# Kernel optimization log

Hardware: AMD Instinct MI355X
Metric: run time of the kernel (lower is better)

The kernel has to match this reference:

```python
import jax, jax.numpy as jnp
import numpy as np
import math

B, TQ, TK, D, H, K = 4, 1024, 1536, 1024, 16, 1
DV = D // H * K  # 64
DP = D * K       # projection dim


def setup_inputs() -> dict:
    key = jax.random.key(0)
    ks = jax.random.split(key, 12)
    s = 0.02
    query = jax.random.normal(ks[0], (B, TQ, D), dtype=jnp.float32)
    key_value = jax.random.normal(ks[1], (B, TK, D), dtype=jnp.float32)
    relative = jax.random.normal(ks[2], (B, TK, D), dtype=jnp.float32)
    # Transformer-XL causal mask: query i may attend to key j <= i + mem
    mem = TK - TQ
    i = jnp.arange(TQ)[:, None]
    j = jnp.arange(TK)[None, :]
    mask = jnp.broadcast_to(j > i + mem, (B, TQ, TK))  # True = masked
    Wq = jax.random.normal(ks[3], (D, DP), dtype=jnp.float32) * s
    Wk = jax.random.normal(ks[4], (D, DP), dtype=jnp.float32) * s
    Wv = jax.random.normal(ks[5], (D, DP), dtype=jnp.float32) * s
    Wr = jax.random.normal(ks[6], (D, DP), dtype=jnp.float32) * s
    Wo = jax.random.normal(ks[7], (DP, D), dtype=jnp.float32) * s
    u = jax.random.normal(ks[8], (DV,), dtype=jnp.float32) * s
    v = jax.random.normal(ks[9], (DV,), dtype=jnp.float32) * s
    gamma = jnp.ones((D,), dtype=jnp.float32)
    beta = jnp.zeros((D,), dtype=jnp.float32)
    return {"query": query, "key_value": key_value, "relative": relative,
            "mask": mask, "Wq": Wq, "Wk": Wk, "Wv": Wv, "Wr": Wr, "Wo": Wo,
            "u": u, "v": v, "gamma": gamma, "beta": beta}


def _layer_norm(x, gamma, beta, eps=1e-5):
    mu = jnp.mean(x, axis=-1, keepdims=True)
    var = jnp.mean(jnp.square(x - mu), axis=-1, keepdims=True)
    return (x - mu) * jax.lax.rsqrt(var + eps) * gamma + beta


def reference(query, key_value, relative, mask, Wq, Wk, Wv, Wr, Wo, u, v, gamma, beta):
    b, tq, d = query.shape
    tk = key_value.shape[1]
    dv = u.shape[0]
    h = Wq.shape[1] // dv
    q = (query @ Wq).reshape(b, tq, h, dv)
    k = (key_value @ Wk).reshape(b, tk, h, dv)
    val = (key_value @ Wv).reshape(b, tk, h, dv)
    r = (relative @ Wr).reshape(b, tk, h, dv)
    # content term (q+u)K^T and position term (q+v)R^T, per head
    ac = jnp.einsum('bqhd,bkhd->bhqk', q + u, k)
    bd = jnp.einsum('bqhd,bkhd->bhqk', q + v, r)
    logits = (ac + bd) * (1.0 / math.sqrt(dv))
    logits = jnp.where(mask[:, None, :, :], -jnp.inf, logits)
    w = jax.nn.softmax(logits, axis=-1)
    ctx = jnp.einsum('bhqk,bkhd->bqhd', w, val).reshape(b, tq, h * dv)
    out = ctx @ Wo + query  # residual
    return _layer_norm(out, gamma, beta)
```

## Files before the change

### kernel.cpp

```cpp
#include <hip/hip_runtime.h>


typedef unsigned short u16;
typedef __attribute__((ext_vector_type(8))) short short8;
typedef __attribute__((ext_vector_type(4))) float floatx4;

#define ATTN_SC 0.18033688011112042f

__device__ __forceinline__ float bf2f(u16 u) {
    union { unsigned int i; float f; } w; w.i = ((unsigned int)u) << 16; return w.f;
}
__device__ __forceinline__ u16 f2bf(float f) {
    union { unsigned int i; float f; } w; w.f = f;
    unsigned int u = w.i;
    return (u16)((u + 0x7FFFu + ((u >> 16) & 1u)) >> 16);
}

__device__ __forceinline__ void gl_lds16(const u16* g, u16* lds) {
    __builtin_amdgcn_global_load_lds(
        (const __attribute__((address_space(1))) void*)g,
        (__attribute__((address_space(3))) void*)lds, 16, 0, 0);
}

__global__ __launch_bounds__(256) void cvt3_kernel(
    const float* __restrict__ x0, u16* __restrict__ y0, int n0,
    const float* __restrict__ x1, u16* __restrict__ y1, int n1,
    const float* __restrict__ x2, u16* __restrict__ y2, int n2)
{
    const int which = blockIdx.y;
    const float* x = (which == 0) ? x0 : (which == 1) ? x1 : x2;
    u16* y         = (which == 0) ? y0 : (which == 1) ? y1 : y2;
    const int n    = (which == 0) ? n0 : (which == 1) ? n1 : n2;
    const int i = (blockIdx.x * 256 + threadIdx.x) * 8;
    if (i >= n) return;
    float4 a = *(const float4*)&x[i];
    float4 b = *(const float4*)&x[i + 4];
    short8 o;
    o[0] = (short)f2bf(a.x); o[1] = (short)f2bf(a.y);
    o[2] = (short)f2bf(a.z); o[3] = (short)f2bf(a.w);
    o[4] = (short)f2bf(b.x); o[5] = (short)f2bf(b.y);
    o[6] = (short)f2bf(b.z); o[7] = (short)f2bf(b.w);
    *(short8*)&y[i] = o;
}

__global__ __launch_bounds__(256) void transpose5_kernel(
    const float* __restrict__ Wq, const float* __restrict__ Wk,
    const float* __restrict__ Wr, const float* __restrict__ Wv,
    const float* __restrict__ Wo,
    u16* __restrict__ WqT, u16* __restrict__ WkrT,
    u16* __restrict__ WvT, u16* __restrict__ WoT)
{
    const int z = blockIdx.z;
    const float* W; u16* WT; int dst_ld, dst_koff;
    switch (z) {
        case 0: W = Wq; WT = WqT;  dst_ld = 1024; dst_koff = 0;    break;
        case 1: W = Wk; WT = WkrT; dst_ld = 2048; dst_koff = 0;    break;
        case 2: W = Wr; WT = WkrT; dst_ld = 2048; dst_koff = 1024; break;
        case 3: W = Wv; WT = WvT;  dst_ld = 1024; dst_koff = 0;    break;
        default:W = Wo; WT = WoT;  dst_ld = 1024; dst_koff = 0;    break;
    }
    __shared__ u16 ts[64][72];
    const int k0 = blockIdx.x * 64, n0 = blockIdx.y * 64;
    const int r  = threadIdx.x >> 2;
    const int c4 = (threadIdx.x & 3) << 4;
    const float* src = &W[(size_t)(k0 + r) * 1024 + n0 + c4];
    for (int j = 0; j < 16; j += 4) {
        float4 a = *(const float4*)(src + j);
        ts[r][c4 + j + 0] = f2bf(a.x);
        ts[r][c4 + j + 1] = f2bf(a.y);
        ts[r][c4 + j + 2] = f2bf(a.z);
        ts[r][c4 + j + 3] = f2bf(a.w);
    }
    __syncthreads();
    short8 t0, t1;
    for (int j = 0; j < 8; j++) t0[j] = (short)ts[c4 + j][r];
    for (int j = 0; j < 8; j++) t1[j] = (short)ts[c4 + 8 + j][r];
    u16* dst = &WT[(size_t)(n0 + r) * dst_ld + dst_koff + k0 + c4];
    *(short8*)dst       = t0;
    *(short8*)(dst + 8) = t1;
}

__global__ __launch_bounds__(256) void wuv_kernel(
    const float* __restrict__ Wk, const float* __restrict__ Wr,
    const float* __restrict__ u, const float* __restrict__ v,
    u16* __restrict__ wuvb)
{
    int idx = blockIdx.x * 256 + threadIdx.x;
    int c = idx >> 4, h = idx & 15;
    float au = 0.f, av = 0.f;
    for (int d = 0; d < 64; d++) {
        au += Wk[(size_t)c * 1024 + h * 64 + d] * u[d];
        av += Wr[(size_t)c * 1024 + h * 64 + d] * v[d];
    }
    wuvb[h * 2048 + c]        = f2bf(au);
    wuvb[h * 2048 + 1024 + c] = f2bf(av);
}

template <int EPI>
__device__ __forceinline__ void gemm_body(
    const u16* __restrict__ A0, const u16* __restrict__ A1,
    const u16* __restrict__ WT, void* __restrict__ out,
    int Kld, int kbeg, int kend, int Ksplit, int T,
    int bm, int bn, u16* As, u16* Ws)
{
    const int tid = threadIdx.x;
    const int wave = tid >> 6, lane = tid & 63;
    const int wm = wave >> 1, wn = wave & 1;
    const int l16 = lane & 15, quad = lane >> 4;

    floatx4 acc[4][4];
    const floatx4 zf = {0.f, 0.f, 0.f, 0.f};
    for (int i = 0; i < 4; i++) for (int j = 0; j < 4; j++) acc[i][j] = zf;

    const int m_base = bm * 128, n_base = bn * 128;
    const int rl = lane >> 2;
    const int cl = (lane & 3) * 8;

    for (int k0 = kbeg; k0 < kend; k0 += 32) {
        const u16* Aptr; int kk;
        if (k0 < Ksplit) { Aptr = A0; kk = k0; } else { Aptr = A1; kk = k0 - Ksplit; }
        __syncthreads();
        for (int half = 0; half < 2; half++) {
            const int r = wave * 32 + half * 16;
            gl_lds16(Aptr + (size_t)(m_base + r + rl) * 1024 + kk + cl, &As[r * 32]);
            gl_lds16(WT   + (size_t)(n_base + r + rl) * Kld  + k0 + cl, &Ws[r * 32]);
        }
        __syncthreads();

        short8 af[4], bf[4];
        for (int i = 0; i < 4; i++) {
            af[i] = *(const short8*)&As[(wm * 64 + i * 16 + l16) * 32 + quad * 8];
            bf[i] = *(const short8*)&Ws[(wn * 64 + i * 16 + l16) * 32 + quad * 8];
        }
        for (int i = 0; i < 4; i++)
            for (int j = 0; j < 4; j++)
                acc[i][j] = __builtin_amdgcn_mfma_f32_16x16x32_bf16(af[i], bf[j], acc[i][j], 0, 0, 0);
    }

    for (int i = 0; i < 4; i++) {
        for (int rg = 0; rg < 4; rg++) {
            const int m = m_base + wm * 64 + i * 16 + quad * 4 + rg;
            float* op = (float*)out;
            for (int j = 0; j < 4; j++) {
                const int col = n_base + wn * 64 + j * 16 + l16;
                op[(size_t)m * 1024 + col] = acc[i][j][rg];
            }
        }
    }
}

__device__ __forceinline__ void stage_half(
    const u16* __restrict__ src, int src_ld, int row_base, int col_base,
    u16* lds_slot, int wave, int lane)
{
    const int r = wave * 16 + (lane >> 2);
    const int c = (((lane & 3) ^ ((lane >> 2) & 3)) << 3);
    gl_lds16(src + (size_t)(row_base + r) * src_ld + col_base + c,
             lds_slot + wave * 512);
    gl_lds16(src + (size_t)(row_base + 128 + r) * src_ld + col_base + c,
             lds_slot + 4096 + wave * 512);
}

template <int EPI, int T>
__device__ __forceinline__ void gemm256_body(
    const u16* __restrict__ A0, const u16* __restrict__ A1,
    const u16* __restrict__ WT, void* __restrict__ out,
    int Kld, int NT, int KsplitTile, int bm, int bn,
    u16* As, u16* Bs)
{
    const int tid  = threadIdx.x;
    const int wave = tid >> 6, lane = tid & 63;
    const int wm = wave >> 2, wn = wave & 3;
    const int l16 = lane & 15, quad = lane >> 4;
    const int m_base = bm * 256, n_base = bn * 256;

    floatx4 acc[8][4];
    const floatx4 zf = {0.f, 0.f, 0.f, 0.f};
    #pragma unroll
    for (int i = 0; i < 8; i++)
        #pragma unroll
        for (int j = 0; j < 4; j++) acc[i][j] = zf;

    {
        const u16* sa0 = (0 < KsplitTile) ? A0 : A1;
        stage_half(sa0, 1024, m_base, 0,  As + 0 * 8192, wave, lane);
        stage_half(WT,  Kld,  n_base, 0,  Bs + 0 * 8192, wave, lane);
        stage_half(sa0, 1024, m_base, 32, As + 1 * 8192, wave, lane);
        stage_half(WT,  Kld,  n_base, 32, Bs + 1 * 8192, wave, lane);
        const u16* sa1 = (1 < KsplitTile) ? A0 : A1;
        const int  c1  = (1 < KsplitTile) ? 64 : (1 - KsplitTile) * 64;
        stage_half(sa1, 1024, m_base, c1, As + 2 * 8192, wave, lane);
        stage_half(WT,  Kld,  n_base, 64, Bs + 2 * 8192, wave, lane);
    }

    for (int t = 0; t < NT; ++t) {
        if (t + 1 < NT) asm volatile("s_waitcnt vmcnt(4)" ::: "memory");
        else            asm volatile("s_waitcnt vmcnt(0)" ::: "memory");
        __builtin_amdgcn_s_barrier();

        short8 bfr[4];
        #pragma unroll
        for (int ph = 0; ph < 4; ++ph) {
            if (ph) __builtin_amdgcn_s_barrier();
            const int ks = ph >> 1, mh = ph & 1;

            if (ph == 0) {
                if (t + 1 < NT) {
                    const int tt = t + 1;
                    const u16* sa = (tt < KsplitTile) ? A0 : A1;
                    const int cb = (tt < KsplitTile ? tt : tt - KsplitTile) * 64 + 32;
                    stage_half(sa, 1024, m_base, cb, As + ((2 * tt + 1) & 3) * 8192, wave, lane);
                }
            } else if (ph == 1) {
                if (t + 1 < NT)
                    stage_half(WT, Kld, n_base, (t + 1) * 64 + 32,
                               Bs + ((2 * (t + 1) + 1) & 3) * 8192, wave, lane);
            } else if (ph == 2) {
                if (t + 2 < NT) {
                    const int tt = t + 2;
                    const u16* sa = (tt < KsplitTile) ? A0 : A1;
                    const int cb = (tt < KsplitTile ? tt : tt - KsplitTile) * 64;
                    stage_half(sa, 1024, m_base, cb, As + ((2 * tt) & 3) * 8192, wave, lane);
                }
            } else {
                if (t + 2 < NT)
                    stage_half(WT, Kld, n_base, (t + 2) * 64,
                               Bs + ((2 * (t + 2)) & 3) * 8192, wave, lane);
            }

            const u16* Aslot = As + ((2 * t + ks) & 3) * 8192;
            const u16* Bslot = Bs + ((2 * t + ks) & 3) * 8192;
            if (mh == 0) {
                #pragma unroll
                for (int nj = 0; nj < 4; ++nj) {
                    const int row = wn * 64 + nj * 16 + l16;
                    bfr[nj] = *(const short8*)&Bslot[row * 32 + (((quad ^ row) & 3) << 3)];
                }
            }
            short8 af[4];
            #pragma unroll
            for (int mi = 0; mi < 4; ++mi) {
                const int row = wm * 128 + mh * 64 + mi * 16 + l16;
                af[mi] = *(const short8*)&Aslot[row * 32 + (((quad ^ row) & 3) << 3)];
            }

            __builtin_amdgcn_s_setprio(1);
            #pragma unroll
            for (int mi = 0; mi < 4; ++mi)
                #pragma unroll
                for (int nj = 0; nj < 4; ++nj)
                    acc[mh * 4 + mi][nj] = __builtin_amdgcn_mfma_f32_16x16x32_bf16(
                        af[mi], bfr[nj], acc[mh * 4 + mi][nj], 0, 0, 0);
            __builtin_amdgcn_s_setprio(0);
        }
    }

    u16* op = (u16*)out;
    #pragma unroll
    for (int mi = 0; mi < 8; ++mi) {
        #pragma unroll
        for (int rg = 0; rg < 4; ++rg) {
            const int m = m_base + wm * 128 + mi * 16 + quad * 4 + rg;
            const int b = m / T, tk = m % T;
            #pragma unroll
            for (int nj = 0; nj < 4; ++nj) {
                const int col = n_base + wn * 64 + nj * 16 + l16;
                const int h = col >> 6, d = col & 63;
                if (EPI == 0) {
                    op[(((size_t)(b * 16 + h) * T + tk) << 6) + d] = f2bf(acc[mi][nj][rg]);
                } else {
                    op[((size_t)(b * 16 + h) * 64 + d) * 1536 + tk] = f2bf(acc[mi][nj][rg]);
                }
            }
        }
    }
}

__device__ __forceinline__ void bias_body8(
    const u16* __restrict__ kvb, const u16* __restrict__ relb,
    const u16* __restrict__ wuvb, float* __restrict__ bias, int bblk)
{
    const int tid = threadIdx.x;
    const int wave = tid >> 6, lane = tid & 63;
    const int l16 = lane & 15, quad = lane >> 4;
    const int tBase = bblk * 128 + wave * 16;

    floatx4 acc = {0.f, 0.f, 0.f, 0.f};
    const u16* arow_kv  = kvb  + (size_t)(tBase + l16) * 1024;
    const u16* arow_rel = relb + (size_t)(tBase + l16) * 1024;
    const u16* brow     = wuvb + (size_t)l16 * 2048;

    for (int ks = 0; ks < 64; ks++) {
        const int k0 = ks * 32;
        const u16* ap = (k0 < 1024) ? (arow_kv + k0) : (arow_rel + k0 - 1024);
        short8 af = *(const short8*)(ap + quad * 8);
        short8 bf = *(const short8*)(brow + k0 + quad * 8);
        acc = __builtin_amdgcn_mfma_f32_16x16x32_bf16(af, bf, acc, 0, 0, 0);
    }
    for (int rg = 0; rg < 4; rg++) {
        const int tg = tBase + quad * 4 + rg;
        const int b = tg / 1536, t = tg % 1536;
        bias[((size_t)b * 16 + l16) * 1536 + t] = acc[rg] * ATTN_SC;
    }
}

__global__ __launch_bounds__(512) void fused_proj_v2(
    const u16* __restrict__ qb, const u16* __restrict__ kvb,
    const u16* __restrict__ relb,
    const u16* __restrict__ WqT, const u16* __restrict__ WkrT,
    const u16* __restrict__ WvT, const u16* __restrict__ wuvb,
    u16* __restrict__ Qh, u16* __restrict__ KRh, u16* __restrict__ Vt,
    float* __restrict__ bias)
{
    __shared__ __align__(128) u16 As[4 * 256 * 32];
    __shared__ __align__(128) u16 Bs[4 * 256 * 32];
    const int blk = blockIdx.x;
    if (blk < 96) {
        gemm256_body<0, 1536>(kvb, relb, WkrT, KRh, 2048, 32, 16,
                              blk % 24, blk / 24, As, Bs);
    } else if (blk < 192) {
        const int i = blk - 96;
        gemm256_body<2, 1536>(kvb, kvb, WvT, Vt, 1024, 16, 99,
                              i % 24, i / 24, As, Bs);
    } else if (blk < 256) {
        const int i = blk - 192;
        gemm256_body<0, 1024>(qb, qb, WqT, Qh, 1024, 16, 99,
                              i % 16, i / 16, As, Bs);
    } else {
        bias_body8(kvb, relb, wuvb, bias, blk - 256);
    }
}

__global__ __launch_bounds__(256) void out_gemm(
    const u16* __restrict__ ctx, const u16* __restrict__ WoT,
    float* __restrict__ outp)
{
    __shared__ u16 smem[2 * 128 * 32];
    const int z = blockIdx.z;
    gemm_body<3>(ctx, nullptr, WoT,
                 outp + (size_t)z * 4 * 1024 * 1024, 1024,
                 z * 512, z * 512 + 512, 1024, 1024,
                 blockIdx.x, blockIdx.y, smem, smem + 128 * 32);
}

__global__ __launch_bounds__(256, 4) void attn_kernel(
    const u16* __restrict__ Qh,
    const u16* __restrict__ KRh,
    const u16* __restrict__ Vt,
    const float* __restrict__ bias,
    u16* __restrict__ ctx)
{
    const int blk  = blockIdx.x;
    const int hb   = blk & 63;
    const int qb   = blk >> 6;
    const int b = hb >> 4, h = hb & 15;
    const int tid = threadIdx.x;
    const int wave = tid >> 6, lane = tid & 63;
    const int l16 = lane & 15, quad = lane >> 4;
    const int qsub = wave >> 1, khalf = wave & 1;
    const int q0 = qb * 64 + qsub * 32;

    const u16* Qp = Qh  + (size_t)hb * 1024 * 64;
    const u16* Kp = KRh + (size_t)hb * 1536 * 64;
    const u16* Vp = Vt  + (size_t)hb * 64 * 1536;
    const float* bp = bias + (size_t)hb * 1536;

    __shared__ u16   Ps[4][2][16][68];
    __shared__ float Obuf[2][2][16][66];
    __shared__ float Lbuf[2][2][16];

    short8 aq[2][2];
    #pragma unroll
    for (int mi = 0; mi < 2; mi++)
        #pragma unroll
        for (int ks = 0; ks < 2; ks++)
            aq[mi][ks] = *(const short8*)
                &Qp[(size_t)(q0 + mi * 16 + l16) * 64 + ks * 32 + quad * 8];

    const floatx4 zf = {0.f, 0.f, 0.f, 0.f};
    floatx4 accO[2][4];
    float lsum[2] = {0.f, 0.f};
    #pragma unroll
    for (int mi = 0; mi < 2; mi++)
        #pragma unroll
        for (int j = 0; j < 4; j++) accO[mi][j] = zf;

    const int nkt = qb + 9;
    for (int kt = khalf; kt < nkt; kt += 2) {
        const int k0 = kt * 64;

        short8 bk[4][2], bv[4][2];
        float4 bc[4];
        #pragma unroll
        for (int n = 0; n < 4; n++)
            #pragma unroll
            for (int ks = 0; ks < 2; ks++)
                bk[n][ks] = *(const short8*)
                    &Kp[(size_t)(k0 + n * 16 + l16) * 64 + ks * 32 + quad * 8];
        #pragma unroll
        for (int j = 0; j < 4; j++)
            #pragma unroll
            for (int ks = 0; ks < 2; ks++)
                bv[j][ks] = *(const short8*)
                    &Vp[(size_t)(j * 16 + l16) * 1536 + k0 + ks * 32 + quad * 8];
        #pragma unroll
        for (int n = 0; n < 4; n++)
            bc[n] = *(const float4*)&bp[k0 + n * 16 + quad * 4];

        #pragma unroll
        for (int mi = 0; mi < 2; mi++) {
            floatx4 accS[4];
            #pragma unroll
            for (int n = 0; n < 4; n++) {
                accS[n] = zf;
                #pragma unroll
                for (int ks = 0; ks < 2; ks++)
                    accS[n] = __builtin_amdgcn_mfma_f32_16x16x32_bf16(
                        bk[n][ks], aq[mi][ks], accS[n], 0, 0, 0);
            }
            const int qg = q0 + mi * 16 + l16;
            const bool domask = (k0 + 63 > q0 + mi * 16 + 512);
            const int lim = qg + 512 - k0;
            #pragma unroll
            for (int n = 0; n < 4; n++) {
                const int limn = lim - n * 16 - quad * 4;
                const float* bcn = (const float*)&bc[n];
                float pv[4];
                #pragma unroll
                for (int rg = 0; rg < 4; rg++) {
                    float s = fmaf(accS[n][rg], ATTN_SC, bcn[rg]);
                    if (domask && rg > limn) s = -1e30f;
                    float pe;
                    asm("v_exp_f32 %0, %1" : "=v"(pe) : "v"(s));
                    lsum[mi] += pe;
                    pv[rg] = pe;
                }
                unsigned w0, w1;
                asm("v_cvt_pk_bf16_f32 %0, %1, %2" : "=v"(w0) : "v"(pv[0]), "v"(pv[1]));
                asm("v_cvt_pk_bf16_f32 %0, %1, %2" : "=v"(w1) : "v"(pv[2]), "v"(pv[3]));
                unsigned* pw = (unsigned*)&Ps[wave][mi][l16][n * 16 + quad * 4];
                pw[0] = w0; pw[1] = w1;
            }
            short8 ap[2];
            #pragma unroll
            for (int ks = 0; ks < 2; ks++)
                ap[ks] = *(const short8*)&Ps[wave][mi][l16][ks * 32 + quad * 8];
            #pragma unroll
            for (int j = 0; j < 4; j++)
                #pragma unroll
                for (int ks = 0; ks < 2; ks++)
                    accO[mi][j] = __builtin_amdgcn_mfma_f32_16x16x32_bf16(
                        ap[ks], bv[j][ks], accO[mi][j], 0, 0, 0);
        }
    }

    #pragma unroll
    for (int mi = 0; mi < 2; mi++) {
        float s = lsum[mi];
        s += __shfl_xor(s, 16, 64);
        s += __shfl_xor(s, 32, 64);
        lsum[mi] = s;
    }

    if (khalf == 1) {
        #pragma unroll
        for (int mi = 0; mi < 2; mi++) {
            #pragma unroll
            for (int j = 0; j < 4; j++)
                #pragma unroll
                for (int rg = 0; rg < 4; rg++)
                    Obuf[qsub][mi][quad * 4 + rg][j * 16 + l16] = accO[mi][j][rg];
            if (quad == 0) Lbuf[qsub][mi][l16] = lsum[mi];
        }
    }
    __syncthreads();
    if (khalf == 0) {
        #pragma unroll
        for (int mi = 0; mi < 2; mi++) {
            const float lt = lsum[mi] + Lbuf[qsub][mi][l16];
            float ltr[4];
            #pragma unroll
            for (int rg = 0; rg < 4; rg++)
                ltr[rg] = __shfl(lt, quad * 4 + rg, 16);
            #pragma unroll
            for (int j = 0; j < 4; j++)
                #pragma unroll
                for (int rg = 0; rg < 4; rg++) {
                    const float o = accO[mi][j][rg]
                                  + Obuf[qsub][mi][quad * 4 + rg][j * 16 + l16];
                    const int q = q0 + mi * 16 + quad * 4 + rg;
                    const int d = j * 16 + l16;
                    ctx[((size_t)b * 1024 + q) * 1024 + h * 64 + d] =
                        f2bf(o / ltr[rg]);
                }
        }
    }
}

__global__ __launch_bounds__(256) void ln_kernel(
    const float* __restrict__ x0, const float* __restrict__ x1,
    const float* __restrict__ q,
    const float* __restrict__ gamma, const float* __restrict__ beta,
    float* __restrict__ out)
{
    const int row = blockIdx.x;
    const int tid = threadIdx.x;
    const size_t base = (size_t)row * 1024 + tid * 4;
    float4 a = *(const float4*)&x0[base];
    float4 c = *(const float4*)&x1[base];
    float4 r = *(const float4*)&q[base];
    float4 v;
    v.x = a.x + c.x + r.x; v.y = a.y + c.y + r.y;
    v.z = a.z + c.z + r.z; v.w = a.w + c.w + r.w;
    float s  = v.x + v.y + v.z + v.w;
    float ss = v.x * v.x + v.y * v.y + v.z * v.z + v.w * v.w;
    for (int off = 1; off < 64; off <<= 1) {
        s  += __shfl_xor(s, off, 64);
        ss += __shfl_xor(ss, off, 64);
    }
    __shared__ float sm[8];
    const int wave = tid >> 6, lane = tid & 63;
    if (lane == 0) { sm[wave] = s; sm[4 + wave] = ss; }
    __syncthreads();
    s  = sm[0] + sm[1] + sm[2] + sm[3];
    ss = sm[4] + sm[5] + sm[6] + sm[7];
    const float mu  = s * (1.f / 1024.f);
    const float var = ss * (1.f / 1024.f) - mu * mu;
    const float inv = rsqrtf(var + 1e-5f);
    float* op = out + (size_t)row * 1024;
    const float* ve = &v.x;
    for (int j = 0; j < 4; j++) {
        const int c2 = tid * 4 + j;
        op[c2] = (ve[j] - mu) * inv * gamma[c2] + beta[c2];
    }
}

extern "C" void kernel_launch(void* const* d_in, const int* in_sizes, int n_in,
                              void* d_out, int out_size, void* d_ws, size_t ws_size,
                              hipStream_t stream)
{
    const float* query     = (const float*)d_in[0];
    const float* key_value = (const float*)d_in[1];
    const float* relative  = (const float*)d_in[2];
    const float* Wq = (const float*)d_in[4];
    const float* Wk = (const float*)d_in[5];
    const float* Wv = (const float*)d_in[6];
    const float* Wr = (const float*)d_in[7];
    const float* Wo = (const float*)d_in[8];
    const float* u  = (const float*)d_in[9];
    const float* v  = (const float*)d_in[10];
    const float* gamma = (const float*)d_in[11];
    const float* beta  = (const float*)d_in[12];

    char* wsp = (char*)d_ws;
    auto alloc = [&](size_t bytes) -> char* {
        char* p = wsp; wsp += (bytes + 255) & ~(size_t)255; return p;
    };
    u16*   qb   = (u16*)alloc((size_t)4 * 1024 * 1024 * 2);
    u16*   kvb  = (u16*)alloc((size_t)4 * 1536 * 1024 * 2);
    u16*   relb = (u16*)alloc((size_t)4 * 1536 * 1024 * 2);
    u16*   WqT  = (u16*)alloc((size_t)1024 * 1024 * 2);
    u16*   WkrT = (u16*)alloc((size_t)1024 * 2048 * 2);
    u16*   WvT  = (u16*)alloc((size_t)1024 * 1024 * 2);
    u16*   WoT  = (u16*)alloc((size_t)1024 * 1024 * 2);
    u16*   wuvb = (u16*)alloc((size_t)16 * 2048 * 2);
    u16*   Qh   = (u16*)alloc((size_t)4 * 16 * 1024 * 64 * 2);
    u16*   KRh  = (u16*)alloc((size_t)4 * 16 * 1536 * 64 * 2);
    u16*   Vt   = (u16*)alloc((size_t)4 * 16 * 64 * 1536 * 2);
    float* bias = (float*)alloc((size_t)4 * 16 * 1536 * 4);
    u16*   ctx  = (u16*)alloc((size_t)4 * 1024 * 1024 * 2);
    float* outp = (float*)alloc((size_t)2 * 4 * 1024 * 1024 * 4);

    const dim3 tb(256);
    cvt3_kernel<<<dim3(3072, 3), tb, 0, stream>>>(
        query, qb, 4 * 1024 * 1024,
        key_value, kvb, 4 * 1536 * 1024,
        relative, relb, 4 * 1536 * 1024);

    transpose5_kernel<<<dim3(16, 16, 5), tb, 0, stream>>>(
        Wq, Wk, Wr, Wv, Wo, WqT, WkrT, WvT, WoT);
    wuv_kernel<<<64, tb, 0, stream>>>(Wk, Wr, u, v, wuvb);

    fused_proj_v2<<<dim3(304), dim3(512), 0, stream>>>(
        qb, kvb, relb, WqT, WkrT, WvT, wuvb, Qh, KRh, Vt, bias);

    attn_kernel<<<dim3(1024), tb, 0, stream>>>(Qh, KRh, Vt, bias, ctx);

    out_gemm<<<dim3(32, 8, 2), tb, 0, stream>>>(ctx, WoT, outp);
    ln_kernel<<<4096, tb, 0, stream>>>(
        outp, outp + (size_t)4 * 1024 * 1024, query, gamma, beta, (float*)d_out);
}
```

Baseline: 336.9 us.

## Stage K/V tiles in swizzled LDS with double-buffered async loads in attention

The attention kernel now has each wave own 16 query rows and walk all key tiles, instead of two waves splitting the key tiles and merging partial outputs through shared memory. Every K and V tile is loaded once per block into XOR-swizzled LDS with global_load_lds and double buffered, so the next tile's load overlaps compute and the four waves no longer each fetch K/V from global memory. The cost is a block-wide barrier every tile. Each wave also now runs twice as many sequential key iterations with a single query row-tile, which lengthens the serial loop per wave.

```diff
diff --git a/kernel.cpp b/kernel.cpp
--- a/kernel.cpp
+++ b/kernel.cpp
@@ -357,144 +357,148 @@
     const int tid = threadIdx.x;
     const int wave = tid >> 6, lane = tid & 63;
     const int l16 = lane & 15, quad = lane >> 4;
-    const int qsub = wave >> 1, khalf = wave & 1;
-    const int q0 = qb * 64 + qsub * 32;
+    const int q0w = qb * 64 + wave * 16;
 
     const u16* Qp = Qh  + (size_t)hb * 1024 * 64;
     const u16* Kp = KRh + (size_t)hb * 1536 * 64;
     const u16* Vp = Vt  + (size_t)hb * 64 * 1536;
     const float* bp = bias + (size_t)hb * 1536;
 
-    __shared__ u16   Ps[4][2][16][68];
-    __shared__ float Obuf[2][2][16][66];
-    __shared__ float Lbuf[2][2][16];
-
-    short8 aq[2][2];
+    __shared__ __align__(128) u16 Kbuf[2][64 * 64];
+    __shared__ __align__(128) u16 Vbuf[2][64 * 64];
+    __shared__ __align__(128) u16 Ps[4][16 * 64];
+
+    const int srow = lane >> 3;
+    const int scol = ((lane & 7) ^ srow) * 8;
+
+    const floatx4 zf = {0.f, 0.f, 0.f, 0.f};
+    floatx4 accO[4];
+    float lsum = 0.f;
     #pragma unroll
-    for (int mi = 0; mi < 2; mi++)
-        #pragma unroll
-        for (int ks = 0; ks < 2; ks++)
-            aq[mi][ks] = *(const short8*)
-                &Qp[(size_t)(q0 + mi * 16 + l16) * 64 + ks * 32 + quad * 8];
-
-    const floatx4 zf = {0.f, 0.f, 0.f, 0.f};
-    floatx4 accO[2][4];
-    float lsum[2] = {0.f, 0.f};
+    for (int j = 0; j < 4; j++) accO[j] = zf;
+
+    short8 aq[2];
     #pragma unroll
-    for (int mi = 0; mi < 2; mi++)
-        #pragma unroll
-        for (int j = 0; j < 4; j++) accO[mi][j] = zf;
+    for (int ks = 0; ks < 2; ks++)
+        aq[ks] = *(const short8*)
+            &Qp[(size_t)(q0w + l16) * 64 + ks * 32 + quad * 8];
 
     const int nkt = qb + 9;
-    for (int kt = khalf; kt < nkt; kt += 2) {
+
+    {
+        const int r0 = wave * 16;
+        gl_lds16(Kp + (size_t)(r0 + srow) * 64 + scol,        &Kbuf[0][r0 * 64]);
+        gl_lds16(Kp + (size_t)(r0 + 8 + srow) * 64 + scol,    &Kbuf[0][(r0 + 8) * 64]);
+        gl_lds16(Vp + (size_t)(r0 + srow) * 1536 + scol,      &Vbuf[0][r0 * 64]);
+        gl_lds16(Vp + (size_t)(r0 + 8 + srow) * 1536 + scol,  &Vbuf[0][(r0 + 8) * 64]);
+    }
+    __syncthreads();
+
+    for (int kt = 0; kt < nkt; kt++) {
         const int k0 = kt * 64;
-
-        short8 bk[4][2], bv[4][2];
+        const int cur = kt & 1;
+
+        if (kt + 1 < nkt) {
+            const int k1 = (kt + 1) * 64;
+            const int r0 = wave * 16;
+            u16* Kd = &Kbuf[cur ^ 1][0];
+            u16* Vd = &Vbuf[cur ^ 1][0];
+            gl_lds16(Kp + (size_t)(k1 + r0 + srow) * 64 + scol,       Kd + r0 * 64);
+            gl_lds16(Kp + (size_t)(k1 + r0 + 8 + srow) * 64 + scol,   Kd + (r0 + 8) * 64);
+            gl_lds16(Vp + (size_t)(r0 + srow) * 1536 + k1 + scol,     Vd + r0 * 64);
+            gl_lds16(Vp + (size_t)(r0 + 8 + srow) * 1536 + k1 + scol, Vd + (r0 + 8) * 64);
+        }
+
         float4 bc[4];
+        #pragma unroll
+        for (int n = 0; n < 4; n++)
+            bc[n] = *(const float4*)&bp[k0 + n * 16 + quad * 4];
+
+        const u16* Kb = &Kbuf[cur][0];
+        const u16* Vb = &Vbuf[cur][0];
+        short8 bk[4][2];
         #pragma unroll
         for (int n = 0; n < 4; n++)
             #pragma unroll
             for (int ks = 0; ks < 2; ks++)
                 bk[n][ks] = *(const short8*)
-                    &Kp[(size_t)(k0 + n * 16 + l16) * 64 + ks * 32 + quad * 8];
-        #pragma unroll
-        for (int j = 0; j < 4; j++)
+                    &Kb[(n * 16 + l16) * 64 + (((ks * 4 + quad) ^ (l16 & 7)) * 8)];
+
+        floatx4 accS[4];
+        #pragma unroll
+        for (int n = 0; n < 4; n++) {
+            accS[n] = zf;
             #pragma unroll
             for (int ks = 0; ks < 2; ks++)
-                bv[j][ks] = *(const short8*)
-                    &Vp[(size_t)(j * 16 + l16) * 1536 + k0 + ks * 32 + quad * 8];
-        #pragma unroll
-        for (int n = 0; n < 4; n++)
-            bc[n] = *(const float4*)&bp[k0 + n * 16 + quad * 4];
-
-        #pragma unroll
-        for (int mi = 0; mi < 2; mi++) {
-            floatx4 accS[4];
-            #pragma unroll
-            for (int n = 0; n < 4; n++) {
-                accS[n] = zf;
-                #pragma unroll
-                for (int ks = 0; ks < 2; ks++)
-                    accS[n] = __builtin_amdgcn_mfma_f32_16x16x32_bf16(
-                        bk[n][ks], aq[mi][ks], accS[n], 0, 0, 0);
-            }
-            const int qg = q0 + mi * 16 + l16;
-            const bool domask = (k0 + 63 > q0 + mi * 16 + 512);
-            const int lim = qg + 512 - k0;
-            #pragma unroll
-            for (int n = 0; n < 4; n++) {
-                const int limn = lim - n * 16 - quad * 4;
-                const float* bcn = (const float*)&bc[n];
-                float pv[4];
-                #pragma unroll
-                for (int rg = 0; rg < 4; rg++) {
-                    float s = fmaf(accS[n][rg], ATTN_SC, bcn[rg]);
-                    if (domask && rg > limn) s = -1e30f;
-                    float pe;
-                    asm("v_exp_f32 %0, %1" : "=v"(pe) : "v"(s));
-                    lsum[mi] += pe;
-                    pv[rg] = pe;
-                }
-                unsigned w0, w1;
-                asm("v_cvt_pk_bf16_f32 %0, %1, %2" : "=v"(w0) : "v"(pv[0]), "v"(pv[1]));
-                asm("v_cvt_pk_bf16_f32 %0, %1, %2" : "=v"(w1) : "v"(pv[2]), "v"(pv[3]));
-                unsigned* pw = (unsigned*)&Ps[wave][mi][l16][n * 16 + quad * 4];
-                pw[0] = w0; pw[1] = w1;
-            }
-            short8 ap[2];
-            #pragma unroll
-            for (int ks = 0; ks < 2; ks++)
-                ap[ks] = *(const short8*)&Ps[wave][mi][l16][ks * 32 + quad * 8];
-            #pragma unroll
-            for (int j = 0; j < 4; j++)
-                #pragma unroll
-                for (int ks = 0; ks < 2; ks++)
-                    accO[mi][j] = __builtin_amdgcn_mfma_f32_16x16x32_bf16(
-                        ap[ks], bv[j][ks], accO[mi][j], 0, 0, 0);
-        }
-    }
-
-    #pragma unroll
-    for (int mi = 0; mi < 2; mi++) {
-        float s = lsum[mi];
+                accS[n] = __builtin_amdgcn_mfma_f32_16x16x32_bf16(
+                    bk[n][ks], aq[ks], accS[n], 0, 0, 0);
+        }
+
+        const int qg = q0w + l16;
+        const bool domask = (k0 + 63 > q0w + 15 + 512);
+        const int lim = qg + 512 - k0;
+        char* Pbase = (char*)&Ps[wave][0];
+        #pragma unroll
+        for (int n = 0; n < 4; n++) {
+            const int limn = lim - n * 16 - quad * 4;
+            const float* bcn = (const float*)&bc[n];
+            float pv[4];
+            #pragma unroll
+            for (int rg = 0; rg < 4; rg++) {
+                float s = fmaf(accS[n][rg], ATTN_SC, bcn[rg]);
+                if (domask && rg > limn) s = -1e30f;
+                float pe;
+                asm("v_exp_f32 %0, %1" : "=v"(pe) : "v"(s));
+                lsum += pe;
+                pv[rg] = pe;
+            }
+            unsigned w0, w1;
+            asm("v_cvt_pk_bf16_f32 %0, %1, %2" : "=v"(w0) : "v"(pv[0]), "v"(pv[1]));
+            asm("v_cvt_pk_bf16_f32 %0, %1, %2" : "=v"(w1) : "v"(pv[2]), "v"(pv[3]));
+            unsigned* pw = (unsigned*)(Pbase +
+                (((l16 * 128 + n * 32 + quad * 8)) ^ ((l16 & 7) << 4)));
+            pw[0] = w0; pw[1] = w1;
+        }
+
+        short8 ap[2];
+        #pragma unroll
+        for (int ks = 0; ks < 2; ks++)
+            ap[ks] = *(const short8*)(Pbase +
+                (((l16 * 128 + ks * 64 + quad * 16)) ^ ((l16 & 7) << 4)));
+        #pragma unroll
+        for (int j = 0; j < 4; j++) {
+            #pragma unroll
+            for (int ks = 0; ks < 2; ks++) {
+                short8 bv = *(const short8*)
+                    &Vb[(j * 16 + l16) * 64 + (((ks * 4 + quad) ^ (l16 & 7)) * 8)];
+                accO[j] = __builtin_amdgcn_mfma_f32_16x16x32_bf16(
+                    ap[ks], bv, accO[j], 0, 0, 0);
+            }
+        }
+
+        __syncthreads();
+    }
+
+    {
+        float s = lsum;
         s += __shfl_xor(s, 16, 64);
         s += __shfl_xor(s, 32, 64);
-        lsum[mi] = s;
-    }
-
-    if (khalf == 1) {
-        #pragma unroll
-        for (int mi = 0; mi < 2; mi++) {
-            #pragma unroll
-            for (int j = 0; j < 4; j++)
-                #pragma unroll
-                for (int rg = 0; rg < 4; rg++)
-                    Obuf[qsub][mi][quad * 4 + rg][j * 16 + l16] = accO[mi][j][rg];
-            if (quad == 0) Lbuf[qsub][mi][l16] = lsum[mi];
-        }
-    }
-    __syncthreads();
-    if (khalf == 0) {
-        #pragma unroll
-        for (int mi = 0; mi < 2; mi++) {
-            const float lt = lsum[mi] + Lbuf[qsub][mi][l16];
-            float ltr[4];
-            #pragma unroll
-            for (int rg = 0; rg < 4; rg++)
-                ltr[rg] = __shfl(lt, quad * 4 + rg, 16);
-            #pragma unroll
-            for (int j = 0; j < 4; j++)
-                #pragma unroll
-                for (int rg = 0; rg < 4; rg++) {
-                    const float o = accO[mi][j][rg]
-                                  + Obuf[qsub][mi][quad * 4 + rg][j * 16 + l16];
-                    const int q = q0 + mi * 16 + quad * 4 + rg;
-                    const int d = j * 16 + l16;
-                    ctx[((size_t)b * 1024 + q) * 1024 + h * 64 + d] =
-                        f2bf(o / ltr[rg]);
-                }
-        }
-    }
+        lsum = s;
+    }
+    float ltr[4];
+    #pragma unroll
+    for (int rg = 0; rg < 4; rg++)
+        ltr[rg] = __shfl(lsum, quad * 4 + rg, 16);
+
+    #pragma unroll
+    for (int j = 0; j < 4; j++)
+        #pragma unroll
+        for (int rg = 0; rg < 4; rg++) {
+            const int q = q0w + quad * 4 + rg;
+            const int d = j * 16 + l16;
+            ctx[((size_t)b * 1024 + q) * 1024 + h * 64 + d] =
+                f2bf(accO[j][rg] / ltr[rg]);
+        }
 }
 
 __global__ __launch_bounds__(256) void ln_kernel(
```

After: 296.7 us. 1.14x faster.
